# Kernel optimization log

Hardware: AMD Instinct MI355X
Metric: run time of the kernel (lower is better)

The kernel has to match this reference:

```python
import jax, jax.numpy as jnp
import numpy as np

N_NODES = 50000
D_IN = 256
D_OUT = 128
N_POS = 1600000   # positive edges used for GCN aggregation
N_PRED = 500000   # edges to score


def setup_inputs() -> dict:
    key = jax.random.key(0)
    ks = jax.random.split(key, 6)
    x = jax.random.normal(ks[0], (N_NODES, D_IN), dtype=jnp.float32)
    pos_edge_index = jax.random.randint(ks[1], (2, N_POS), 0, N_NODES)
    edge_index = jax.random.randint(ks[2], (2, N_PRED), 0, N_NODES)
    # init_linear: Linear(d_in, d_in); stored as (in, out) so fwd is x @ W1 + b1
    W1 = jax.random.normal(ks[3], (D_IN, D_IN), dtype=jnp.float32) / np.sqrt(D_IN).astype(np.float32)
    b1 = jnp.zeros((D_IN,), dtype=jnp.float32)
    # GCNConv weight (in, out) and bias
    Wc = jax.random.normal(ks[4], (D_IN, D_OUT), dtype=jnp.float32) / np.sqrt(D_IN).astype(np.float32)
    bc = jnp.zeros((D_OUT,), dtype=jnp.float32)
    return dict(x=x, edge_index=edge_index, pos_edge_index=pos_edge_index,
                W1=W1, b1=b1, Wc=Wc, bc=bc)


def reference(x, edge_index, pos_edge_index, W1, b1, Wc, bc):
    n = x.shape[0]
    # init_linear
    h = x @ W1 + b1                                  # [N, D_IN]
    # GCNConv: linear transform first, then normalized scatter-add aggregation
    h = h @ Wc                                       # [N, D_OUT]
    # add self-loops (PyG GCNConv default add_self_loops=True, edge_weight=1)
    loops = jnp.arange(n, dtype=pos_edge_index.dtype)
    row = jnp.concatenate([pos_edge_index[0], loops])  # source
    col = jnp.concatenate([pos_edge_index[1], loops])  # target (aggregation)
    # symmetric normalization: deg over target, norm = d^-1/2[row]*d^-1/2[col]
    deg = jax.ops.segment_sum(jnp.ones_like(col, dtype=h.dtype), col, num_segments=n)
    dinv = jnp.where(deg > 0, jax.lax.rsqrt(deg), 0.0)
    norm = dinv[row] * dinv[col]                     # [E+N]
    msgs = h[row] * norm[:, None]                    # gather + scale
    out = jax.ops.segment_sum(msgs, col, num_segments=n) + bc  # scatter-add + bias
    # edge dot-product scoring
    logits = (out[edge_index[0]] * out[edge_index[1]]).sum(axis=-1)  # [N_PRED]
    return logits
```

## Files before the change

kernel.cpp:

```cpp
#include <hip/hip_runtime.h>

#define N_NODES 50000
#define D_IN 256
#define D_OUT 128
#define N_POS 1600000
#define N_PRED 500000

#define G_BUCKETS 782
#define GPAD 1024
#define SB 640
#define CHUNK 2500
#define CAP 4096
#define GEMM_BLOCKS 782

typedef __attribute__((ext_vector_type(8))) short short8;
typedef __attribute__((ext_vector_type(4))) float f32x4;

__device__ __forceinline__ unsigned short f2bf(float f) {
    unsigned int u = __float_as_uint(f);
    u += 0x7FFFu + ((u >> 16) & 1u);
    return (unsigned short)(u >> 16);
}
__device__ __forceinline__ unsigned int pk2(float a, float b) {
    unsigned int ua = __float_as_uint(a), ub = __float_as_uint(b);
    ua += 0x7FFFu + ((ua >> 16) & 1u);
    ub += 0x7FFFu + ((ub >> 16) & 1u);
    return (ua >> 16) | (ub & 0xFFFF0000u);
}
__device__ __forceinline__ float bflo(unsigned int u) { return __uint_as_float(u << 16); }
__device__ __forceinline__ float bfhi(unsigned int u) { return __uint_as_float(u & 0xFFFF0000u); }

__global__ void fuse_weights_k(const float* __restrict__ W1, const float* __restrict__ Wc,
                               const float* __restrict__ b1,
                               unsigned short* __restrict__ Bp, float* __restrict__ bf,
                               int* __restrict__ bfill) {
    if (blockIdx.x == 128) {
        for (int g = threadIdx.x; g < G_BUCKETS; g += 256) bfill[g] = g * CAP;
        return;
    }
    int gid = blockIdx.x * blockDim.x + threadIdx.x;
    int k = gid >> 7;
    int n = gid & 127;
    float acc = 0.f;
    #pragma unroll 4
    for (int kk = 0; kk < D_IN; ++kk)
        acc += W1[k * D_IN + kk] * Wc[kk * D_OUT + n];
    int ks = k >> 5, q = (k >> 3) & 3, jj = k & 7;
    int nt = n >> 4, nl = n & 15;
    int lane = q * 16 + nl;
    Bp[(((long)(ks * 8 + nt)) * 64 + lane) * 8 + jj] = f2bf(acc);
    if (gid < D_OUT) {
        float accb = 0.f;
        for (int kk = 0; kk < D_IN; ++kk)
            accb += b1[kk] * Wc[kk * D_OUT + gid];
        bf[gid] = accb;
    }
}

__global__ __launch_bounds__(256) void scatter_gemm_k(const int* __restrict__ row,
                                                      const int* __restrict__ col,
                                                      int* __restrict__ bfill,
                                                      unsigned int* __restrict__ eb,
                                                      const float* __restrict__ x,
                                                      const uint4* __restrict__ Bp,
                                                      const float* __restrict__ bf,
                                                      unsigned short* __restrict__ hsb) {
    __shared__ __align__(16) char smem[27456];
    if (blockIdx.x < GEMM_BLOCKS) {
        const int wave = threadIdx.x >> 6;
        const int lane = threadIdx.x & 63;
        const int q    = lane >> 4;
        const int ml   = lane & 15;
        const int m0   = blockIdx.x * 64 + wave * 16;

        f32x4 acc[8];
        #pragma unroll
        for (int t = 0; t < 8; ++t) acc[t] = (f32x4){0.f, 0.f, 0.f, 0.f};

        long arow = m0 + ml; if (arow > N_NODES - 1) arow = N_NODES - 1;
        const float* xrow = x + arow * D_IN + q * 8;

        #pragma unroll
        for (int ks = 0; ks < 8; ++ks) {
            float4 xa = *(const float4*)(xrow + ks * 32);
            float4 xb = *(const float4*)(xrow + ks * 32 + 4);
            union { short8 s; unsigned int u[4]; } af;
            af.u[0] = pk2(xa.x, xa.y);
            af.u[1] = pk2(xa.z, xa.w);
            af.u[2] = pk2(xb.x, xb.y);
            af.u[3] = pk2(xb.z, xb.w);
            #pragma unroll
            for (int nt = 0; nt < 8; ++nt) {
                union { uint4 v; short8 s; } bu;
                bu.v = Bp[(long)(ks * 8 + nt) * 64 + lane];
                acc[nt] = __builtin_amdgcn_mfma_f32_16x16x32_bf16(af.s, bu.s, acc[nt], 0, 0, 0);
            }
        }

        unsigned short* o = (unsigned short*)smem + wave * 2048;
        #pragma unroll
        for (int nt = 0; nt < 8; ++nt) {
            float bn = bf[nt * 16 + ml];
            #pragma unroll
            for (int r = 0; r < 4; ++r) {
                float val = acc[nt][r] + bn;
                o[(q * 4 + r) * 128 + nt * 16 + ml] = f2bf(val);
            }
        }
        __syncthreads();
        #pragma unroll
        for (int i = 0; i < 4; ++i) {
            int fb = i * 1024 + lane * 16;
            int v = m0 + (fb >> 8);
            if (v < N_NODES) {
                uint4 val = *(const uint4*)((const char*)o + fb);
                *(uint4*)((char*)hsb + (long)v * 256 + (fb & 255)) = val;
            }
        }
    } else {
        int* hist  = (int*)smem;
        int* lofs  = hist + GPAD;
        int* fill2 = lofs + GPAD;
        int* base  = fill2 + GPAD;
        int* part  = base + GPAD;
        unsigned int* stag = (unsigned int*)(part + 256);
        int t = threadIdx.x;
        for (int i = t; i < GPAD; i += 256) { hist[i] = 0; fill2[i] = 0; }
        __syncthreads();
        int e0 = (blockIdx.x - GEMM_BLOCKS) * CHUNK;
        for (int i = t; i < CHUNK; i += 256)
            atomicAdd(&hist[col[e0 + i] >> 6], 1);
        __syncthreads();
        int h[4], p4 = 0;
        #pragma unroll
        for (int i = 0; i < 4; ++i) { h[i] = hist[4 * t + i]; p4 += h[i]; }
        part[t] = p4;
        __syncthreads();
        for (int d = 1; d < 256; d <<= 1) {
            int add = (t >= d) ? part[t - d] : 0;
            __syncthreads();
            part[t] += add;
            __syncthreads();
        }
        int ex = part[t] - p4;
        #pragma unroll
        for (int i = 0; i < 4; ++i) { lofs[4 * t + i] = ex; ex += h[i]; }
        __syncthreads();
        for (int g = t; g < G_BUCKETS; g += 256) {
            int c = hist[g];
            base[g] = c ? atomicAdd(&bfill[g], c) : 0;
        }
        for (int i = t; i < CHUNK; i += 256) {
            int c = col[e0 + i];
            int g = c >> 6;
            unsigned int u = (unsigned int)row[e0 + i] | ((unsigned int)(c & 63) << 16)
                           | ((unsigned int)g << 22);
            int lp = atomicAdd(&fill2[g], 1);
            stag[lofs[g] + lp] = u;
        }
        __syncthreads();
        for (int i = t; i < CHUNK; i += 256) {
            unsigned int u = stag[i];
            int g = u >> 22;
            eb[base[g] + (i - lofs[g])] = u;
        }
    }
}

__global__ __launch_bounds__(256) void csr_build_k(const int* __restrict__ bfill,
                                                   const unsigned int* __restrict__ eb,
                                                   unsigned short* __restrict__ csr,
                                                   int* __restrict__ offs,
                                                   int* __restrict__ ends,
                                                   float* __restrict__ dinv) {
    __shared__ unsigned int stag[CAP];
    __shared__ unsigned short stag2[CAP];
    __shared__ int hist[64], lofs[64], fill[64];
    int t = threadIdx.x;
    int g = blockIdx.x;
    int s = g * CAP;
    int cnt = bfill[g] - s;
    if (t < 64) { hist[t] = 0; fill[t] = 0; }
    __syncthreads();
    for (int i = t; i < cnt; i += 256) {
        unsigned int u = eb[s + i];
        stag[i] = u;
        atomicAdd(&hist[(u >> 16) & 63], 1);
    }
    __syncthreads();
    if (t == 0) {
        int run = 0;
        for (int k = 0; k < 64; ++k) { lofs[k] = run; run += hist[k]; }
    }
    __syncthreads();
    if (t < 64) {
        int v = g * 64 + t;
        if (v < N_NODES) {
            offs[v] = s + lofs[t];
            ends[v] = s + lofs[t] + hist[t];
            dinv[v] = rsqrtf((float)hist[t] + 1.0f);
        }
    }
    for (int i = t; i < cnt; i += 256) {
        unsigned int u = stag[i];
        int nl = (u >> 16) & 63;
        int lp = atomicAdd(&fill[nl], 1);
        stag2[lofs[nl] + lp] = (unsigned short)(u & 0xFFFF);
    }
    __syncthreads();
    for (int i = t; i < cnt; i += 256)
        csr[s + i] = stag2[i];
}

__global__ __launch_bounds__(256) void aggregate_csr_k(const int* __restrict__ offs,
                                                       const int* __restrict__ ends,
                                                       const unsigned short* __restrict__ csr,
                                                       const uint4* __restrict__ hs4,
                                                       const float* __restrict__ dinv,
                                                       const float* __restrict__ bc,
                                                       uint4* __restrict__ feat4) {
    int v    = blockIdx.x * 4 + (threadIdx.x >> 6);
    int lane = threadIdx.x & 63;
    int grp  = lane >> 4, li = lane & 15;
    int s0 = offs[v], s1 = ends[v];

    float a[8] = {0.f, 0.f, 0.f, 0.f, 0.f, 0.f, 0.f, 0.f};
    int i = s0 + grp;
    for (; i + 4 < s1; i += 8) {
        int r0 = csr[i], r1 = csr[i + 4];
        uint4 u0 = hs4[r0 * 16 + li];
        uint4 u1 = hs4[r1 * 16 + li];
        float d0 = dinv[r0], d1 = dinv[r1];
        a[0] = fmaf(d0, bflo(u0.x), a[0]); a[0] = fmaf(d1, bflo(u1.x), a[0]);
        a[1] = fmaf(d0, bfhi(u0.x), a[1]); a[1] = fmaf(d1, bfhi(u1.x), a[1]);
        a[2] = fmaf(d0, bflo(u0.y), a[2]); a[2] = fmaf(d1, bflo(u1.y), a[2]);
        a[3] = fmaf(d0, bfhi(u0.y), a[3]); a[3] = fmaf(d1, bfhi(u1.y), a[3]);
        a[4] = fmaf(d0, bflo(u0.z), a[4]); a[4] = fmaf(d1, bflo(u1.z), a[4]);
        a[5] = fmaf(d0, bfhi(u0.z), a[5]); a[5] = fmaf(d1, bfhi(u1.z), a[5]);
        a[6] = fmaf(d0, bflo(u0.w), a[6]); a[6] = fmaf(d1, bflo(u1.w), a[6]);
        a[7] = fmaf(d0, bfhi(u0.w), a[7]); a[7] = fmaf(d1, bfhi(u1.w), a[7]);
    }
    if (i < s1) {
        int r = csr[i];
        uint4 u = hs4[r * 16 + li];
        float d = dinv[r];
        a[0] = fmaf(d, bflo(u.x), a[0]); a[1] = fmaf(d, bfhi(u.x), a[1]);
        a[2] = fmaf(d, bflo(u.y), a[2]); a[3] = fmaf(d, bfhi(u.y), a[3]);
        a[4] = fmaf(d, bflo(u.z), a[4]); a[5] = fmaf(d, bfhi(u.z), a[5]);
        a[6] = fmaf(d, bflo(u.w), a[6]); a[7] = fmaf(d, bfhi(u.w), a[7]);
    }
    #pragma unroll
    for (int j = 0; j < 8; ++j) {
        a[j] += __shfl_xor(a[j], 16);
        a[j] += __shfl_xor(a[j], 32);
    }
    if (grp == 0) {
        uint4 su = hs4[v * 16 + li];
        float dv = dinv[v];
        float4 b0 = *(const float4*)(bc + li * 8);
        float4 b1 = *(const float4*)(bc + li * 8 + 4);
        float f0 = dv * (a[0] + dv * bflo(su.x)) + b0.x;
        float f1 = dv * (a[1] + dv * bfhi(su.x)) + b0.y;
        float f2 = dv * (a[2] + dv * bflo(su.y)) + b0.z;
        float f3 = dv * (a[3] + dv * bfhi(su.y)) + b0.w;
        float f4 = dv * (a[4] + dv * bflo(su.z)) + b1.x;
        float f5 = dv * (a[5] + dv * bfhi(su.z)) + b1.y;
        float f6 = dv * (a[6] + dv * bflo(su.w)) + b1.z;
        float f7 = dv * (a[7] + dv * bfhi(su.w)) + b1.w;
        uint4 o;
        o.x = pk2(f0, f1); o.y = pk2(f2, f3); o.z = pk2(f4, f5); o.w = pk2(f6, f7);
        feat4[v * 16 + li] = o;
    }
}

__global__ void score_k(const int* __restrict__ src, const int* __restrict__ dst,
                        const uint4* __restrict__ feat4, float* __restrict__ out) {
    int gid = blockIdx.x * blockDim.x + threadIdx.x;
    int e = gid >> 4;
    int c = gid & 15;
    if (e >= N_PRED) return;
    int a = src[e], b = dst[e];
    uint4 ua = feat4[(long)a * 16 + c];
    uint4 ub = feat4[(long)b * 16 + c];
    float p = bflo(ua.x) * bflo(ub.x) + bfhi(ua.x) * bfhi(ub.x)
            + bflo(ua.y) * bflo(ub.y) + bfhi(ua.y) * bfhi(ub.y)
            + bflo(ua.z) * bflo(ub.z) + bfhi(ua.z) * bfhi(ub.z)
            + bflo(ua.w) * bflo(ub.w) + bfhi(ua.w) * bfhi(ub.w);
    #pragma unroll
    for (int m = 8; m; m >>= 1) p += __shfl_xor(p, m, 16);
    if (c == 0) out[e] = p;
}

extern "C" void kernel_launch(void* const* d_in, const int* in_sizes, int n_in,
                              void* d_out, int out_size, void* d_ws, size_t ws_size,
                              hipStream_t stream) {
    const float* x   = (const float*)d_in[0];
    const int*   ei  = (const int*)  d_in[1];
    const int*   pe  = (const int*)  d_in[2];
    const float* W1  = (const float*)d_in[3];
    const float* b1  = (const float*)d_in[4];
    const float* Wc  = (const float*)d_in[5];
    const float* bc  = (const float*)d_in[6];
    float* out = (float*)d_out;

    const int* pe_row = pe;
    const int* pe_col = pe + N_POS;
    const int* ei_src = ei;
    const int* ei_dst = ei + N_PRED;

    char* w = (char*)d_ws;
    unsigned short* Bp = (unsigned short*)w;  w += 32768 * 2;
    float* bf    = (float*)w;                 w += 128 * 4;
    float* dinv  = (float*)w;                 w += 50000 * 4;
    int*   bfill = (int*)w;                   w += GPAD * 4;
    int*   offs  = (int*)w;                   w += 50000 * 4;
    int*   ends  = (int*)w;                   w += 50000 * 4;
    unsigned int* eb = (unsigned int*)w;      w += (long)G_BUCKETS * CAP * 4;
    unsigned short* csr = (unsigned short*)w; w += (long)G_BUCKETS * CAP * 2;
    unsigned short* hsb   = (unsigned short*)w;  w += (long)N_NODES * D_OUT * 2;
    unsigned short* featb = (unsigned short*)w;

    fuse_weights_k<<<129, 256, 0, stream>>>(W1, Wc, b1, Bp, bf, bfill);

    scatter_gemm_k<<<GEMM_BLOCKS + SB, 256, 0, stream>>>(pe_row, pe_col, bfill, eb,
                                                         x, (const uint4*)Bp, bf, hsb);

    csr_build_k   <<<G_BUCKETS, 256, 0, stream>>>(bfill, eb, csr, offs, ends, dinv);

    aggregate_csr_k<<<N_NODES / 4, 256, 0, stream>>>(offs, ends, csr, (const uint4*)hsb,
                                                     dinv, bc, (uint4*)featb);

    score_k       <<<(int)(((long)N_PRED * 16) / 256), 256, 0, stream>>>(
                      ei_src, ei_dst, (const uint4*)featb, out);
}
```

Measured before the change: 267.8 us.

## Fuse all five stages into one persistent cooperative kernel with grid syncs

Replaces the five separate kernel launches with a single cooperative persistent kernel. The blocks loop over the former grid domains, and grid.sync() stands in for the boundaries between kernels. The goal is to remove launch overhead and the inter-kernel gaps. In exchange, occupancy is limited by the union shared-memory footprint and launch bounds, each grid-wide barrier has its own cost, and the persistent loops lose the GEMM and scatter overlap that a larger grid gave.

```diff
diff --git a/kernel.cpp b/kernel.cpp
--- a/kernel.cpp
+++ b/kernel.cpp
@@ -1,4 +1,7 @@
 #include <hip/hip_runtime.h>
+#include <hip/hip_cooperative_groups.h>
+
+namespace cg = cooperative_groups;
 
 #define N_NODES 50000
 #define D_IN 256
@@ -7,7 +10,6 @@
 #define N_PRED 500000
 
 #define G_BUCKETS 782
-#define GPAD 1024
 #define SB 640
 #define CHUNK 2500
 #define CAP 4096
@@ -30,265 +32,273 @@
 __device__ __forceinline__ float bflo(unsigned int u) { return __uint_as_float(u << 16); }
 __device__ __forceinline__ float bfhi(unsigned int u) { return __uint_as_float(u & 0xFFFF0000u); }
 
-__global__ void fuse_weights_k(const float* __restrict__ W1, const float* __restrict__ Wc,
-                               const float* __restrict__ b1,
-                               unsigned short* __restrict__ Bp, float* __restrict__ bf,
-                               int* __restrict__ bfill) {
-    if (blockIdx.x == 128) {
-        for (int g = threadIdx.x; g < G_BUCKETS; g += 256) bfill[g] = g * CAP;
-        return;
-    }
-    int gid = blockIdx.x * blockDim.x + threadIdx.x;
-    int k = gid >> 7;
-    int n = gid & 127;
-    float acc = 0.f;
-    #pragma unroll 4
-    for (int kk = 0; kk < D_IN; ++kk)
-        acc += W1[k * D_IN + kk] * Wc[kk * D_OUT + n];
-    int ks = k >> 5, q = (k >> 3) & 3, jj = k & 7;
-    int nt = n >> 4, nl = n & 15;
-    int lane = q * 16 + nl;
-    Bp[(((long)(ks * 8 + nt)) * 64 + lane) * 8 + jj] = f2bf(acc);
-    if (gid < D_OUT) {
-        float accb = 0.f;
-        for (int kk = 0; kk < D_IN; ++kk)
-            accb += b1[kk] * Wc[kk * D_OUT + gid];
-        bf[gid] = accb;
-    }
-}
-
-__global__ __launch_bounds__(256) void scatter_gemm_k(const int* __restrict__ row,
-                                                      const int* __restrict__ col,
-                                                      int* __restrict__ bfill,
-                                                      unsigned int* __restrict__ eb,
-                                                      const float* __restrict__ x,
-                                                      const uint4* __restrict__ Bp,
-                                                      const float* __restrict__ bf,
-                                                      unsigned short* __restrict__ hsb) {
-    __shared__ __align__(16) char smem[27456];
-    if (blockIdx.x < GEMM_BLOCKS) {
-        const int wave = threadIdx.x >> 6;
-        const int lane = threadIdx.x & 63;
-        const int q    = lane >> 4;
-        const int ml   = lane & 15;
-        const int m0   = blockIdx.x * 64 + wave * 16;
-
-        f32x4 acc[8];
-        #pragma unroll
-        for (int t = 0; t < 8; ++t) acc[t] = (f32x4){0.f, 0.f, 0.f, 0.f};
-
-        long arow = m0 + ml; if (arow > N_NODES - 1) arow = N_NODES - 1;
-        const float* xrow = x + arow * D_IN + q * 8;
-
-        #pragma unroll
-        for (int ks = 0; ks < 8; ++ks) {
-            float4 xa = *(const float4*)(xrow + ks * 32);
-            float4 xb = *(const float4*)(xrow + ks * 32 + 4);
-            union { short8 s; unsigned int u[4]; } af;
-            af.u[0] = pk2(xa.x, xa.y);
-            af.u[1] = pk2(xa.z, xa.w);
-            af.u[2] = pk2(xb.x, xb.y);
-            af.u[3] = pk2(xb.z, xb.w);
+struct P {
+    const int* rows; const int* cols;
+    const float* x; const float* W1; const float* b1;
+    const float* Wc; const float* bc;
+    const int* esrc; const int* edst; float* out;
+    unsigned short* Bp; float* bf; int* bfill;
+    int* offs; int* ends; float* dinv;
+    unsigned int* eb; unsigned short* csr;
+    unsigned short* hsb; unsigned short* featb;
+};
+
+union SM {
+    struct {
+        int hist[G_BUCKETS]; int lofs[G_BUCKETS]; int fill2[G_BUCKETS];
+        int base[G_BUCKETS]; int part[256]; unsigned int stag[CHUNK];
+    } sc;
+    struct {
+        unsigned short ot[4][2048];
+    } ge;
+    struct {
+        unsigned int stag[CAP]; unsigned short stag2[CAP];
+        int hist[64]; int lofs[64]; int fill[64];
+    } cb;
+};
+
+__global__ __launch_bounds__(256, 4) void mega_k(P p) {
+    __shared__ SM sm;
+    cg::grid_group grid = cg::this_grid();
+    const int t = threadIdx.x;
+
+    for (int vb = blockIdx.x; vb <= 128; vb += gridDim.x) {
+        if (vb == 128) {
+            for (int g = t; g < G_BUCKETS; g += 256) p.bfill[g] = g * CAP;
+        } else {
+            int gid = vb * 256 + t;
+            int k = gid >> 7, n = gid & 127;
+            float acc = 0.f;
+            #pragma unroll 4
+            for (int kk = 0; kk < D_IN; ++kk)
+                acc += p.W1[k * D_IN + kk] * p.Wc[kk * D_OUT + n];
+            int ks = k >> 5, q = (k >> 3) & 3, jj = k & 7;
+            int nt = n >> 4, nl = n & 15;
+            int lane = q * 16 + nl;
+            p.Bp[(((long)(ks * 8 + nt)) * 64 + lane) * 8 + jj] = f2bf(acc);
+            if (gid < D_OUT) {
+                float accb = 0.f;
+                for (int kk = 0; kk < D_IN; ++kk)
+                    accb += p.b1[kk] * p.Wc[kk * D_OUT + gid];
+                p.bf[gid] = accb;
+            }
+        }
+    }
+    grid.sync();
+
+    for (int wk = blockIdx.x; wk < GEMM_BLOCKS + SB; wk += gridDim.x) {
+        __syncthreads();
+        if (wk < GEMM_BLOCKS) {
+            const int wave = t >> 6, lane = t & 63;
+            const int q = lane >> 4, ml = lane & 15;
+            const int m0 = wk * 64 + wave * 16;
+            f32x4 acc[8];
+            #pragma unroll
+            for (int i = 0; i < 8; ++i) acc[i] = (f32x4){0.f, 0.f, 0.f, 0.f};
+            long arow = m0 + ml; if (arow > N_NODES - 1) arow = N_NODES - 1;
+            const float* xrow = p.x + arow * D_IN + q * 8;
+            const uint4* Bp4 = (const uint4*)p.Bp;
+            #pragma unroll
+            for (int ks = 0; ks < 8; ++ks) {
+                float4 xa = *(const float4*)(xrow + ks * 32);
+                float4 xb = *(const float4*)(xrow + ks * 32 + 4);
+                union { short8 s; unsigned int u[4]; } af;
+                af.u[0] = pk2(xa.x, xa.y);
+                af.u[1] = pk2(xa.z, xa.w);
+                af.u[2] = pk2(xb.x, xb.y);
+                af.u[3] = pk2(xb.z, xb.w);
+                #pragma unroll
+                for (int nt = 0; nt < 8; ++nt) {
+                    union { uint4 v; short8 s; } bu;
+                    bu.v = Bp4[(long)(ks * 8 + nt) * 64 + lane];
+                    acc[nt] = __builtin_amdgcn_mfma_f32_16x16x32_bf16(af.s, bu.s, acc[nt], 0, 0, 0);
+                }
+            }
+            unsigned short* o = sm.ge.ot[wave];
             #pragma unroll
             for (int nt = 0; nt < 8; ++nt) {
-                union { uint4 v; short8 s; } bu;
-                bu.v = Bp[(long)(ks * 8 + nt) * 64 + lane];
-                acc[nt] = __builtin_amdgcn_mfma_f32_16x16x32_bf16(af.s, bu.s, acc[nt], 0, 0, 0);
-            }
-        }
-
-        unsigned short* o = (unsigned short*)smem + wave * 2048;
-        #pragma unroll
-        for (int nt = 0; nt < 8; ++nt) {
-            float bn = bf[nt * 16 + ml];
-            #pragma unroll
-            for (int r = 0; r < 4; ++r) {
-                float val = acc[nt][r] + bn;
-                o[(q * 4 + r) * 128 + nt * 16 + ml] = f2bf(val);
-            }
-        }
-        __syncthreads();
-        #pragma unroll
-        for (int i = 0; i < 4; ++i) {
-            int fb = i * 1024 + lane * 16;
-            int v = m0 + (fb >> 8);
+                float bn = p.bf[nt * 16 + ml];
+                #pragma unroll
+                for (int r = 0; r < 4; ++r)
+                    o[(q * 4 + r) * 128 + nt * 16 + ml] = f2bf(acc[nt][r] + bn);
+            }
+            __syncthreads();
+            #pragma unroll
+            for (int i = 0; i < 4; ++i) {
+                int fb = i * 1024 + lane * 16;
+                int v = m0 + (fb >> 8);
+                if (v < N_NODES) {
+                    uint4 val = *(const uint4*)((const char*)o + fb);
+                    *(uint4*)((char*)p.hsb + (long)v * 256 + (fb & 255)) = val;
+                }
+            }
+        } else {
+            int* hist  = sm.sc.hist;  int* lofs = sm.sc.lofs;
+            int* fill2 = sm.sc.fill2; int* base = sm.sc.base;
+            int* part  = sm.sc.part;  unsigned int* stag = sm.sc.stag;
+            for (int i = t; i < G_BUCKETS; i += 256) { hist[i] = 0; fill2[i] = 0; }
+            __syncthreads();
+            int e0 = (wk - GEMM_BLOCKS) * CHUNK;
+            for (int i = t; i < CHUNK; i += 256)
+                atomicAdd(&hist[p.cols[e0 + i] >> 6], 1);
+            __syncthreads();
+            int h[4], p4 = 0;
+            #pragma unroll
+            for (int i = 0; i < 4; ++i) {
+                int idx = 4 * t + i;
+                h[i] = (idx < G_BUCKETS) ? hist[idx] : 0;
+                p4 += h[i];
+            }
+            part[t] = p4;
+            __syncthreads();
+            for (int d = 1; d < 256; d <<= 1) {
+                int add = (t >= d) ? part[t - d] : 0;
+                __syncthreads();
+                part[t] += add;
+                __syncthreads();
+            }
+            int ex = part[t] - p4;
+            #pragma unroll
+            for (int i = 0; i < 4; ++i) {
+                int idx = 4 * t + i;
+                if (idx < G_BUCKETS) lofs[idx] = ex;
+                ex += h[i];
+            }
+            __syncthreads();
+            for (int g = t; g < G_BUCKETS; g += 256) {
+                int c = hist[g];
+                base[g] = c ? atomicAdd(&p.bfill[g], c) : 0;
+            }
+            for (int i = t; i < CHUNK; i += 256) {
+                int c = p.cols[e0 + i];
+                int g = c >> 6;
+                unsigned int u = (unsigned int)p.rows[e0 + i]
+                               | ((unsigned int)(c & 63) << 16) | ((unsigned int)g << 22);
+                int lp = atomicAdd(&fill2[g], 1);
+                stag[lofs[g] + lp] = u;
+            }
+            __syncthreads();
+            for (int i = t; i < CHUNK; i += 256) {
+                unsigned int u = stag[i];
+                int g = u >> 22;
+                p.eb[base[g] + (i - lofs[g])] = u;
+            }
+        }
+    }
+    grid.sync();
+
+    for (int g = blockIdx.x; g < G_BUCKETS; g += gridDim.x) {
+        __syncthreads();
+        int s = g * CAP;
+        int cnt = p.bfill[g] - s;
+        if (t < 64) { sm.cb.hist[t] = 0; sm.cb.fill[t] = 0; }
+        __syncthreads();
+        for (int i = t; i < cnt; i += 256) {
+            unsigned int u = p.eb[s + i];
+            sm.cb.stag[i] = u;
+            atomicAdd(&sm.cb.hist[(u >> 16) & 63], 1);
+        }
+        __syncthreads();
+        if (t == 0) {
+            int run = 0;
+            for (int k = 0; k < 64; ++k) { sm.cb.lofs[k] = run; run += sm.cb.hist[k]; }
+        }
+        __syncthreads();
+        if (t < 64) {
+            int v = g * 64 + t;
             if (v < N_NODES) {
-                uint4 val = *(const uint4*)((const char*)o + fb);
-                *(uint4*)((char*)hsb + (long)v * 256 + (fb & 255)) = val;
-            }
-        }
-    } else {
-        int* hist  = (int*)smem;
-        int* lofs  = hist + GPAD;
-        int* fill2 = lofs + GPAD;
-        int* base  = fill2 + GPAD;
-        int* part  = base + GPAD;
-        unsigned int* stag = (unsigned int*)(part + 256);
-        int t = threadIdx.x;
-        for (int i = t; i < GPAD; i += 256) { hist[i] = 0; fill2[i] = 0; }
-        __syncthreads();
-        int e0 = (blockIdx.x - GEMM_BLOCKS) * CHUNK;
-        for (int i = t; i < CHUNK; i += 256)
-            atomicAdd(&hist[col[e0 + i] >> 6], 1);
-        __syncthreads();
-        int h[4], p4 = 0;
-        #pragma unroll
-        for (int i = 0; i < 4; ++i) { h[i] = hist[4 * t + i]; p4 += h[i]; }
-        part[t] = p4;
-        __syncthreads();
-        for (int d = 1; d < 256; d <<= 1) {
-            int add = (t >= d) ? part[t - d] : 0;
-            __syncthreads();
-            part[t] += add;
-            __syncthreads();
-        }
-        int ex = part[t] - p4;
-        #pragma unroll
-        for (int i = 0; i < 4; ++i) { lofs[4 * t + i] = ex; ex += h[i]; }
-        __syncthreads();
-        for (int g = t; g < G_BUCKETS; g += 256) {
-            int c = hist[g];
-            base[g] = c ? atomicAdd(&bfill[g], c) : 0;
-        }
-        for (int i = t; i < CHUNK; i += 256) {
-            int c = col[e0 + i];
-            int g = c >> 6;
-            unsigned int u = (unsigned int)row[e0 + i] | ((unsigned int)(c & 63) << 16)
-                           | ((unsigned int)g << 22);
-            int lp = atomicAdd(&fill2[g], 1);
-            stag[lofs[g] + lp] = u;
-        }
-        __syncthreads();
-        for (int i = t; i < CHUNK; i += 256) {
-            unsigned int u = stag[i];
-            int g = u >> 22;
-            eb[base[g] + (i - lofs[g])] = u;
-        }
-    }
-}
-
-__global__ __launch_bounds__(256) void csr_build_k(const int* __restrict__ bfill,
-                                                   const unsigned int* __restrict__ eb,
-                                                   unsigned short* __restrict__ csr,
-                                                   int* __restrict__ offs,
-                                                   int* __restrict__ ends,
-                                                   float* __restrict__ dinv) {
-    __shared__ unsigned int stag[CAP];
-    __shared__ unsigned short stag2[CAP];
-    __shared__ int hist[64], lofs[64], fill[64];
-    int t = threadIdx.x;
-    int g = blockIdx.x;
-    int s = g * CAP;
-    int cnt = bfill[g] - s;
-    if (t < 64) { hist[t] = 0; fill[t] = 0; }
-    __syncthreads();
-    for (int i = t; i < cnt; i += 256) {
-        unsigned int u = eb[s + i];
-        stag[i] = u;
-        atomicAdd(&hist[(u >> 16) & 63], 1);
-    }
-    __syncthreads();
-    if (t == 0) {
-        int run = 0;
-        for (int k = 0; k < 64; ++k) { lofs[k] = run; run += hist[k]; }
-    }
-    __syncthreads();
-    if (t < 64) {
-        int v = g * 64 + t;
-        if (v < N_NODES) {
-            offs[v] = s + lofs[t];
-            ends[v] = s + lofs[t] + hist[t];
-            dinv[v] = rsqrtf((float)hist[t] + 1.0f);
-        }
-    }
-    for (int i = t; i < cnt; i += 256) {
-        unsigned int u = stag[i];
-        int nl = (u >> 16) & 63;
-        int lp = atomicAdd(&fill[nl], 1);
-        stag2[lofs[nl] + lp] = (unsigned short)(u & 0xFFFF);
-    }
-    __syncthreads();
-    for (int i = t; i < cnt; i += 256)
-        csr[s + i] = stag2[i];
-}
-
-__global__ __launch_bounds__(256) void aggregate_csr_k(const int* __restrict__ offs,
-                                                       const int* __restrict__ ends,
-                                                       const unsigned short* __restrict__ csr,
-                                                       const uint4* __restrict__ hs4,
-                                                       const float* __restrict__ dinv,
-                                                       const float* __restrict__ bc,
-                                                       uint4* __restrict__ feat4) {
-    int v    = blockIdx.x * 4 + (threadIdx.x >> 6);
-    int lane = threadIdx.x & 63;
-    int grp  = lane >> 4, li = lane & 15;
-    int s0 = offs[v], s1 = ends[v];
-
-    float a[8] = {0.f, 0.f, 0.f, 0.f, 0.f, 0.f, 0.f, 0.f};
-    int i = s0 + grp;
-    for (; i + 4 < s1; i += 8) {
-        int r0 = csr[i], r1 = csr[i + 4];
-        uint4 u0 = hs4[r0 * 16 + li];
-        uint4 u1 = hs4[r1 * 16 + li];
-        float d0 = dinv[r0], d1 = dinv[r1];
-        a[0] = fmaf(d0, bflo(u0.x), a[0]); a[0] = fmaf(d1, bflo(u1.x), a[0]);
-        a[1] = fmaf(d0, bfhi(u0.x), a[1]); a[1] = fmaf(d1, bfhi(u1.x), a[1]);
-        a[2] = fmaf(d0, bflo(u0.y), a[2]); a[2] = fmaf(d1, bflo(u1.y), a[2]);
-        a[3] = fmaf(d0, bfhi(u0.y), a[3]); a[3] = fmaf(d1, bfhi(u1.y), a[3]);
-        a[4] = fmaf(d0, bflo(u0.z), a[4]); a[4] = fmaf(d1, bflo(u1.z), a[4]);
-        a[5] = fmaf(d0, bfhi(u0.z), a[5]); a[5] = fmaf(d1, bfhi(u1.z), a[5]);
-        a[6] = fmaf(d0, bflo(u0.w), a[6]); a[6] = fmaf(d1, bflo(u1.w), a[6]);
-        a[7] = fmaf(d0, bfhi(u0.w), a[7]); a[7] = fmaf(d1, bfhi(u1.w), a[7]);
-    }
-    if (i < s1) {
-        int r = csr[i];
-        uint4 u = hs4[r * 16 + li];
-        float d = dinv[r];
-        a[0] = fmaf(d, bflo(u.x), a[0]); a[1] = fmaf(d, bfhi(u.x), a[1]);
-        a[2] = fmaf(d, bflo(u.y), a[2]); a[3] = fmaf(d, bfhi(u.y), a[3]);
-        a[4] = fmaf(d, bflo(u.z), a[4]); a[5] = fmaf(d, bfhi(u.z), a[5]);
-        a[6] = fmaf(d, bflo(u.w), a[6]); a[7] = fmaf(d, bfhi(u.w), a[7]);
-    }
-    #pragma unroll
-    for (int j = 0; j < 8; ++j) {
-        a[j] += __shfl_xor(a[j], 16);
-        a[j] += __shfl_xor(a[j], 32);
-    }
-    if (grp == 0) {
-        uint4 su = hs4[v * 16 + li];
-        float dv = dinv[v];
-        float4 b0 = *(const float4*)(bc + li * 8);
-        float4 b1 = *(const float4*)(bc + li * 8 + 4);
-        float f0 = dv * (a[0] + dv * bflo(su.x)) + b0.x;
-        float f1 = dv * (a[1] + dv * bfhi(su.x)) + b0.y;
-        float f2 = dv * (a[2] + dv * bflo(su.y)) + b0.z;
-        float f3 = dv * (a[3] + dv * bfhi(su.y)) + b0.w;
-        float f4 = dv * (a[4] + dv * bflo(su.z)) + b1.x;
-        float f5 = dv * (a[5] + dv * bfhi(su.z)) + b1.y;
-        float f6 = dv * (a[6] + dv * bflo(su.w)) + b1.z;
-        float f7 = dv * (a[7] + dv * bfhi(su.w)) + b1.w;
-        uint4 o;
-        o.x = pk2(f0, f1); o.y = pk2(f2, f3); o.z = pk2(f4, f5); o.w = pk2(f6, f7);
-        feat4[v * 16 + li] = o;
-    }
-}
-
-__global__ void score_k(const int* __restrict__ src, const int* __restrict__ dst,
-                        const uint4* __restrict__ feat4, float* __restrict__ out) {
-    int gid = blockIdx.x * blockDim.x + threadIdx.x;
-    int e = gid >> 4;
-    int c = gid & 15;
-    if (e >= N_PRED) return;
-    int a = src[e], b = dst[e];
-    uint4 ua = feat4[(long)a * 16 + c];
-    uint4 ub = feat4[(long)b * 16 + c];
-    float p = bflo(ua.x) * bflo(ub.x) + bfhi(ua.x) * bfhi(ub.x)
-            + bflo(ua.y) * bflo(ub.y) + bfhi(ua.y) * bfhi(ub.y)
-            + bflo(ua.z) * bflo(ub.z) + bfhi(ua.z) * bfhi(ub.z)
-            + bflo(ua.w) * bflo(ub.w) + bfhi(ua.w) * bfhi(ub.w);
-    #pragma unroll
-    for (int m = 8; m; m >>= 1) p += __shfl_xor(p, m, 16);
-    if (c == 0) out[e] = p;
+                p.offs[v] = s + sm.cb.lofs[t];
+                p.ends[v] = s + sm.cb.lofs[t] + sm.cb.hist[t];
+                p.dinv[v] = rsqrtf((float)sm.cb.hist[t] + 1.0f);
+            }
+        }
+        for (int i = t; i < cnt; i += 256) {
+            unsigned int u = sm.cb.stag[i];
+            int nl = (u >> 16) & 63;
+            int lp = atomicAdd(&sm.cb.fill[nl], 1);
+            sm.cb.stag2[sm.cb.lofs[nl] + lp] = (unsigned short)(u & 0xFFFF);
+        }
+        __syncthreads();
+        for (int i = t; i < cnt; i += 256)
+            p.csr[s + i] = sm.cb.stag2[i];
+    }
+    grid.sync();
+
+    {
+        const uint4* hs4 = (const uint4*)p.hsb;
+        uint4* feat4 = (uint4*)p.featb;
+        int lane = t & 63, grp = lane >> 4, li = lane & 15;
+        for (int vb = blockIdx.x; vb < N_NODES / 4; vb += gridDim.x) {
+            int v = vb * 4 + (t >> 6);
+            int s0 = p.offs[v], s1 = p.ends[v];
+            float a[8] = {0.f, 0.f, 0.f, 0.f, 0.f, 0.f, 0.f, 0.f};
+            int i = s0 + grp;
+            for (; i + 4 < s1; i += 8) {
+                int r0 = p.csr[i], r1 = p.csr[i + 4];
+                uint4 u0 = hs4[r0 * 16 + li];
+                uint4 u1 = hs4[r1 * 16 + li];
+                float d0 = p.dinv[r0], d1 = p.dinv[r1];
+                a[0] = fmaf(d0, bflo(u0.x), a[0]); a[0] = fmaf(d1, bflo(u1.x), a[0]);
+                a[1] = fmaf(d0, bfhi(u0.x), a[1]); a[1] = fmaf(d1, bfhi(u1.x), a[1]);
+                a[2] = fmaf(d0, bflo(u0.y), a[2]); a[2] = fmaf(d1, bflo(u1.y), a[2]);
+                a[3] = fmaf(d0, bfhi(u0.y), a[3]); a[3] = fmaf(d1, bfhi(u1.y), a[3]);
+                a[4] = fmaf(d0, bflo(u0.z), a[4]); a[4] = fmaf(d1, bflo(u1.z), a[4]);
+                a[5] = fmaf(d0, bfhi(u0.z), a[5]); a[5] = fmaf(d1, bfhi(u1.z), a[5]);
+                a[6] = fmaf(d0, bflo(u0.w), a[6]); a[6] = fmaf(d1, bflo(u1.w), a[6]);
+                a[7] = fmaf(d0, bfhi(u0.w), a[7]); a[7] = fmaf(d1, bfhi(u1.w), a[7]);
+            }
+            if (i < s1) {
+                int r = p.csr[i];
+                uint4 u = hs4[r * 16 + li];
+                float d = p.dinv[r];
+                a[0] = fmaf(d, bflo(u.x), a[0]); a[1] = fmaf(d, bfhi(u.x), a[1]);
+                a[2] = fmaf(d, bflo(u.y), a[2]); a[3] = fmaf(d, bfhi(u.y), a[3]);
+                a[4] = fmaf(d, bflo(u.z), a[4]); a[5] = fmaf(d, bfhi(u.z), a[5]);
+                a[6] = fmaf(d, bflo(u.w), a[6]); a[7] = fmaf(d, bfhi(u.w), a[7]);
+            }
+            #pragma unroll
+            for (int j = 0; j < 8; ++j) {
+                a[j] += __shfl_xor(a[j], 16);
+                a[j] += __shfl_xor(a[j], 32);
+            }
+            if (grp == 0) {
+                uint4 su = hs4[v * 16 + li];
+                float dv = p.dinv[v];
+                float4 b0 = *(const float4*)(p.bc + li * 8);
+                float4 b1 = *(const float4*)(p.bc + li * 8 + 4);
+                float f0 = dv * (a[0] + dv * bflo(su.x)) + b0.x;
+                float f1 = dv * (a[1] + dv * bfhi(su.x)) + b0.y;
+                float f2 = dv * (a[2] + dv * bflo(su.y)) + b0.z;
+                float f3 = dv * (a[3] + dv * bfhi(su.y)) + b0.w;
+                float f4 = dv * (a[4] + dv * bflo(su.z)) + b1.x;
+                float f5 = dv * (a[5] + dv * bfhi(su.z)) + b1.y;
+                float f6 = dv * (a[6] + dv * bflo(su.w)) + b1.z;
+                float f7 = dv * (a[7] + dv * bfhi(su.w)) + b1.w;
+                uint4 o;
+                o.x = pk2(f0, f1); o.y = pk2(f2, f3); o.z = pk2(f4, f5); o.w = pk2(f6, f7);
+                feat4[v * 16 + li] = o;
+            }
+        }
+    }
+    grid.sync();
+
+    {
+        const uint4* feat4 = (const uint4*)p.featb;
+        for (int vb = blockIdx.x; vb < (N_PRED * 16) / 256; vb += gridDim.x) {
+            int gid = vb * 256 + t;
+            int e = gid >> 4, c = gid & 15;
+            int a = p.esrc[e], b = p.edst[e];
+            uint4 ua = feat4[(long)a * 16 + c];
+            uint4 ub = feat4[(long)b * 16 + c];
+            float pr = bflo(ua.x) * bflo(ub.x) + bfhi(ua.x) * bfhi(ub.x)
+                     + bflo(ua.y) * bflo(ub.y) + bfhi(ua.y) * bfhi(ub.y)
+                     + bflo(ua.z) * bflo(ub.z) + bfhi(ua.z) * bfhi(ub.z)
+                     + bflo(ua.w) * bflo(ub.w) + bfhi(ua.w) * bfhi(ub.w);
+            #pragma unroll
+            for (int m = 8; m; m >>= 1) pr += __shfl_xor(pr, m, 16);
+            if (c == 0) p.out[e] = pr;
+        }
+    }
 }
 
 extern "C" void kernel_launch(void* const* d_in, const int* in_sizes, int n_in,
@@ -301,18 +311,12 @@
     const float* b1  = (const float*)d_in[4];
     const float* Wc  = (const float*)d_in[5];
     const float* bc  = (const float*)d_in[6];
-    float* out = (float*)d_out;
-
-    const int* pe_row = pe;
-    const int* pe_col = pe + N_POS;
-    const int* ei_src = ei;
-    const int* ei_dst = ei + N_PRED;
 
     char* w = (char*)d_ws;
     unsigned short* Bp = (unsigned short*)w;  w += 32768 * 2;
     float* bf    = (float*)w;                 w += 128 * 4;
     float* dinv  = (float*)w;                 w += 50000 * 4;
-    int*   bfill = (int*)w;                   w += GPAD * 4;
+    int*   bfill = (int*)w;                   w += 1024 * 4;
     int*   offs  = (int*)w;                   w += 50000 * 4;
     int*   ends  = (int*)w;                   w += 50000 * 4;
     unsigned int* eb = (unsigned int*)w;      w += (long)G_BUCKETS * CAP * 4;
@@ -320,16 +324,21 @@
     unsigned short* hsb   = (unsigned short*)w;  w += (long)N_NODES * D_OUT * 2;
     unsigned short* featb = (unsigned short*)w;
 
-    fuse_weights_k<<<129, 256, 0, stream>>>(W1, Wc, b1, Bp, bf, bfill);
-
-    scatter_gemm_k<<<GEMM_BLOCKS + SB, 256, 0, stream>>>(pe_row, pe_col, bfill, eb,
-                                                         x, (const uint4*)Bp, bf, hsb);
-
-    csr_build_k   <<<G_BUCKETS, 256, 0, stream>>>(bfill, eb, csr, offs, ends, dinv);
-
-    aggregate_csr_k<<<N_NODES / 4, 256, 0, stream>>>(offs, ends, csr, (const uint4*)hsb,
-                                                     dinv, bc, (uint4*)featb);
-
-    score_k       <<<(int)(((long)N_PRED * 16) / 256), 256, 0, stream>>>(
-                      ei_src, ei_dst, (const uint4*)featb, out);
+    P p;
+    p.rows = pe;             p.cols = pe + N_POS;
+    p.x = x; p.W1 = W1; p.b1 = b1; p.Wc = Wc; p.bc = bc;
+    p.esrc = ei;             p.edst = ei + N_PRED;
+    p.out = (float*)d_out;
+    p.Bp = Bp; p.bf = bf; p.bfill = bfill;
+    p.offs = offs; p.ends = ends; p.dinv = dinv;
+    p.eb = eb; p.csr = csr; p.hsb = hsb; p.featb = featb;
+
+    int occ = 0;
+    hipOccupancyMaxActiveBlocksPerMultiprocessor(&occ, mega_k, 256, 0);
+    if (occ < 1) occ = 1;
+    if (occ > 8) occ = 8;
+    int grid = occ * 256;
+
+    void* args[] = { &p };
+    hipLaunchCooperativeKernel((void*)mega_k, dim3(grid), dim3(256), args, 0, stream);
 }
```

Result: slower. 609.5 us (+127.6%).
